# Kernel optimization log

Measured on AMD Instinct MI355X. Metric: run time of the kernel, lower is better.

The kernel has to match this reference:

```python
import jax, jax.numpy as jnp
import numpy as np

BQ = 64  # query block size
BK = 64  # key block size
PV_SCALE = 1e-3  # pvthreshd (~0..50) -> prob threshold, mirrors int8 P-quantization cutoff


def setup_inputs() -> dict:
    key = jax.random.key(0)
    ks = jax.random.split(key, 6)
    B, H, L, D = 2, 16, 2048, 64
    q = jax.random.normal(ks[0], (B, H, L, D), jnp.float32)
    k = jax.random.normal(ks[1], (B, H, L, D), jnp.float32)
    v = jax.random.normal(ks[2], (B, H, L, D), jnp.float32)
    # per-head tuned thresholds (init defaults / autotune ranges)
    cdfthreshd = 0.85 + 0.14 * jax.random.uniform(ks[3], (H,), jnp.float32)
    simthreshd1 = jax.random.uniform(ks[4], (H,), jnp.float32, minval=-0.3, maxval=0.5)
    pvthreshd = jax.random.uniform(ks[5], (H,), jnp.float32, minval=15.0, maxval=25.0)
    return dict(q=q, k=k, v=v, cdfthreshd=cdfthreshd,
                simthreshd1=simthreshd1, pvthreshd=pvthreshd)


def _sparse_meansim_attention(q, k, v, cdfthreshd, simthreshd1, pvthreshd):
    B, H, L, D = q.shape
    nqb, nkb = L // BQ, L // BK
    scale = 1.0 / jnp.sqrt(jnp.float32(D))

    # smooth_k: subtract per-(B,H) key mean along sequence
    k = k - k.mean(axis=2, keepdims=True)

    qb = q.reshape(B, H, nqb, BQ, D)
    kb = k.reshape(B, H, nkb, BK, D)
    qm = qb.mean(axis=3)  # [B,H,nqb,D]
    km = kb.mean(axis=3)  # [B,H,nkb,D]

    # mean cosine similarity of queries to their block mean -> pooled (prunable) blocks
    qn = jnp.linalg.norm(qb, axis=-1)            # [B,H,nqb,BQ]
    qmn = jnp.linalg.norm(qm, axis=-1)           # [B,H,nqb]
    cos = jnp.einsum('bhnqd,bhnd->bhnq', qb, qm) / (qn * qmn[..., None] + 1e-6)
    pooled = cos.mean(axis=-1) > simthreshd1[None, :, None]  # [B,H,nqb]

    # block-level score map from pooled means, CDF-based top-mass block selection
    s = jnp.einsum('bhid,bhjd->bhij', qm, km) * scale        # [B,H,nqb,nkb]
    p = jax.nn.softmax(s, axis=-1)
    order = jnp.argsort(-p, axis=-1)
    p_sorted = jnp.take_along_axis(p, order, axis=-1)
    excl_cdf = jnp.cumsum(p_sorted, axis=-1) - p_sorted      # exclusive CDF
    keep_sorted = excl_cdf < cdfthreshd[None, :, None, None]
    keep = jnp.take_along_axis(keep_sorted, jnp.argsort(order, axis=-1), axis=-1)

    sink = (jnp.arange(nkb) == 0)  # attention_sink: always keep first key block
    block_mask = keep | (~pooled)[..., None] | sink          # [B,H,nqb,nkb]

    # full attention restricted to selected blocks
    S = jnp.einsum('bhqd,bhkd->bhqk', q, k) * scale          # [B,H,L,L]
    m = jnp.repeat(jnp.repeat(block_mask, BQ, axis=2), BK, axis=3)
    P = jax.nn.softmax(jnp.where(m, S, -jnp.inf), axis=-1)

    # second-stage PV pruning: skip PV accumulation for negligible prob blocks
    Pb = P.reshape(B, H, nqb, BQ, nkb, BK)
    pv_keep = Pb.max(axis=(3, 5)) >= pvthreshd[None, :, None, None] * PV_SCALE
    pv_keep = pv_keep | sink
    Pb = Pb * pv_keep[:, :, :, None, :, None].astype(P.dtype)

    o = jnp.einsum('bhqk,bhkd->bhqd', Pb.reshape(B, H, L, L), v)
    return o


def reference(q, k, v, cdfthreshd, simthreshd1, pvthreshd):
    return _sparse_meansim_attention(q, k, v, cdfthreshd, simthreshd1, pvthreshd)
```

## Files before the change

kernel.cpp:

```cpp
#include <hip/hip_runtime.h>
#include <hip/hip_bf16.h>
#include <math.h>
#include <stdint.h>

#define B 2
#define H 16
#define L 2048
#define D 64
#define NB 32

typedef unsigned short u16;
typedef unsigned int u32;
typedef __attribute__((ext_vector_type(2))) unsigned int u32x2;
typedef __attribute__((ext_vector_type(4))) unsigned int u32x4;
typedef __attribute__((ext_vector_type(8))) short s16x8;
typedef __attribute__((ext_vector_type(4))) float f32x4;

union FragU { s16x8 v; u32 u[4]; };

__device__ __forceinline__ u32 pkbf(float a, float b) {
  __hip_bfloat162 h = __float22bfloat162_rn(make_float2(a, b));
  union { __hip_bfloat162 h; u32 u; } cv; cv.h = h; return cv.u;
}
__device__ __forceinline__ float bf2f(u32 u16bits) {
  union { u32 u; float f; } c; c.u = u16bits << 16; return c.f;
}
__device__ __forceinline__ void split4(float4 p, u32x2& hi, u32x2& lo) {
  u32 h01 = pkbf(p.x, p.y), h23 = pkbf(p.z, p.w);
  float rx = p.x - bf2f(h01 & 0xffffu);
  float ry = p.y - bf2f(h01 >> 16);
  float rz = p.z - bf2f(h23 & 0xffffu);
  float rw = p.w - bf2f(h23 >> 16);
  hi = (u32x2){h01, h23};
  lo = (u32x2){pkbf(rx, ry), pkbf(rz, rw)};
}
__device__ __forceinline__ int swz(int row, int colb) {
  return (row << 7) + (colb ^ ((row & 7) << 4));
}

__global__ __launch_bounds__(256) void k_prep(const float* __restrict__ k,
                                              const float* __restrict__ v,
                                              float* __restrict__ ksum,
                                              u16* __restrict__ khi_g,
                                              u16* __restrict__ klo_g,
                                              u16* __restrict__ vthi_g,
                                              u16* __restrict__ vtlo_g,
                                              float* __restrict__ kbmax) {
  int blk = blockIdx.x, bh = blk >> 5, j = blk & 31, t = threadIdx.x;
  int lane = t & 63, w = t >> 6;
  __shared__ float vt[64 * 65];
  __shared__ float pk_[4][64];
  __shared__ unsigned bmaxS;
  if (t == 0) bmaxS = 0u;
  size_t base = (size_t)blk * 4096;

  int r0 = t >> 3;
  int c8 = (t & 7) * 8;
  float cs[8] = {0.f, 0.f, 0.f, 0.f, 0.f, 0.f, 0.f, 0.f};
  float rmax = 0.f;
#pragma unroll
  for (int it = 0; it < 2; ++it) {
    int r = r0 + 32 * it;
    const float* kp = k + base + r * 64 + c8;
    float4 f0 = *(const float4*)kp;
    float4 f1 = *(const float4*)(kp + 4);
    u32x2 h0, l0, h1, l1;
    split4(f0, h0, l0); split4(f1, h1, l1);
    *(u32x4*)(khi_g + base + r * 64 + c8) = (u32x4){h0[0], h0[1], h1[0], h1[1]};
    *(u32x4*)(klo_g + base + r * 64 + c8) = (u32x4){l0[0], l0[1], l1[0], l1[1]};
    cs[0] += f0.x; cs[1] += f0.y; cs[2] += f0.z; cs[3] += f0.w;
    cs[4] += f1.x; cs[5] += f1.y; cs[6] += f1.z; cs[7] += f1.w;
    float ssq = f0.x*f0.x + f0.y*f0.y + f0.z*f0.z + f0.w*f0.w
              + f1.x*f1.x + f1.y*f1.y + f1.z*f1.z + f1.w*f1.w;
    ssq += __shfl_xor(ssq, 1); ssq += __shfl_xor(ssq, 2); ssq += __shfl_xor(ssq, 4);
    if ((t & 7) == 0) rmax = fmaxf(rmax, ssq);
    const float* vp = v + base + r * 64 + c8;
    float4 g0 = *(const float4*)vp;
    float4 g1 = *(const float4*)(vp + 4);
    vt[(c8 + 0) * 65 + r] = g0.x;
    vt[(c8 + 1) * 65 + r] = g0.y;
    vt[(c8 + 2) * 65 + r] = g0.z;
    vt[(c8 + 3) * 65 + r] = g0.w;
    vt[(c8 + 4) * 65 + r] = g1.x;
    vt[(c8 + 5) * 65 + r] = g1.y;
    vt[(c8 + 6) * 65 + r] = g1.z;
    vt[(c8 + 7) * 65 + r] = g1.w;
  }
  if ((t & 7) == 0) atomicMax(&bmaxS, __float_as_uint(rmax));
#pragma unroll
  for (int i = 0; i < 8; ++i) {
    cs[i] += __shfl_xor(cs[i], 8);
    cs[i] += __shfl_xor(cs[i], 16);
    cs[i] += __shfl_xor(cs[i], 32);
  }
  if (lane < 8) {
    *(float4*)&pk_[w][lane * 8]     = (float4){cs[0], cs[1], cs[2], cs[3]};
    *(float4*)&pk_[w][lane * 8 + 4] = (float4){cs[4], cs[5], cs[6], cs[7]};
  }
  __syncthreads();
  if (t < 64) ksum[(size_t)blk * 64 + t] = pk_[0][t] + pk_[1][t] + pk_[2][t] + pk_[3][t];
  if (t == 0) kbmax[blk] = __uint_as_float(bmaxS);
#pragma unroll
  for (int it = 0; it < 2; ++it) {
    int idx = t + 256 * it, d = idx >> 3, s8 = (idx & 7) * 8;
    const float* vr = &vt[d * 65 + s8];
    float4 f0 = {vr[0], vr[1], vr[2], vr[3]};
    float4 f1 = {vr[4], vr[5], vr[6], vr[7]};
    u32x2 h0, l0, h1, l1;
    split4(f0, h0, l0); split4(f1, h1, l1);
    size_t o = (size_t)bh * 131072 + (size_t)d * 2048 + j * 64 + s8;
    *(u32x4*)(vthi_g + o) = (u32x4){h0[0], h0[1], h1[0], h1[1]};
    *(u32x4*)(vtlo_g + o) = (u32x4){l0[0], l0[1], l1[0], l1[1]};
  }
}

__global__ __launch_bounds__(256, 3) void k_attn(
    const float* __restrict__ q,
    const float* __restrict__ ksum,
    const u16* __restrict__ khi_g, const u16* __restrict__ klo_g,
    const u16* __restrict__ vthi_g, const u16* __restrict__ vtlo_g,
    const float* __restrict__ cdfthreshd, const float* __restrict__ simthreshd1,
    const float* __restrict__ pvthreshd, const float* __restrict__ kbmax,
    float* __restrict__ out) {
  int blk0 = blockIdx.x;
  int blk = (blk0 & 7) * 128 + (blk0 >> 3);
  int bh = blk >> 5, iq = blk & 31, h = bh & (H - 1);
  int t = threadIdx.x, lane = t & 63, w = t >> 6;
  int m16 = lane & 15, quad = lane >> 4;

  __shared__ __align__(16) uint8_t smem[24608];
  uint8_t* phB = smem;
  uint8_t* plB = smem + 8192;
  uint8_t* qloB = smem + 16384;
  u32*   rbm   = (u32*)smem;
  float* lpart = (float*)(smem + 8448);
  float* qmS   = (float*)(smem + 9472);
  float* MSs   = (float*)(smem + 9728);
  float* linvS = (float*)(smem + 9984);
  int*   flg   = (int*)(smem + 24576);

  const float* qg = q + ((size_t)bh * L + (size_t)iq * 64) * D;
  const u16* kh = khi_g + (size_t)bh * (L * D);
  const u16* kl = klo_g + (size_t)bh * (L * D);
  const u16* vh = vthi_g + (size_t)bh * (L * D);
  const u16* vl = vtlo_g + (size_t)bh * (L * D);

  s16x8 qhf[4][2];
#pragma unroll
  for (int nt = 0; nt < 4; ++nt)
#pragma unroll
    for (int ks = 0; ks < 2; ++ks) {
      const float* p0 = qg + (size_t)(16 * nt + m16) * 64 + ks * 32 + quad * 8;
      float4 a = *(const float4*)p0;
      float4 b2 = *(const float4*)(p0 + 4);
      u32x2 ha, la, hb, lb;
      split4(a, ha, la); split4(b2, hb, lb);
      FragU fh;
      fh.u[0] = ha[0]; fh.u[1] = ha[1]; fh.u[2] = hb[0]; fh.u[3] = hb[1];
      qhf[nt][ks] = fh.v;
      if (w == 0)
        *(u32x4*)(qloB + swz(16 * nt + m16, ks * 64 + quad * 16)) =
            (u32x4){la[0], la[1], lb[0], lb[1]};
    }
  for (int e = t; e < 64 * 33; e += 256) rbm[e] = 0x7F800000u;

  if (w == 0) {
    float s = 0.f;
    for (int r = 0; r < 64; ++r) s += qg[r * 64 + lane];
    qmS[lane] = s * (1.f / 64.f);
  }
  if (w == 1) {
    float m = (lane < 32) ? kbmax[bh * 32 + lane] : 0.f;
    for (int off = 16; off; off >>= 1) m = fmaxf(m, __shfl_xor(m, off, 32));
    if (lane == 0) ((float*)flg)[3] = m;
  }
  __syncthreads();

  bool keepj = false;
  if (w == 0 && lane < 32) {
    int j = lane;
    const float* ksp = ksum + (size_t)bh * NB * 64 + j * 64;
    float sv = 0.f;
    for (int d = 0; d < 64; ++d) sv += qmS[d] * ksp[d];
    sv *= (1.f / 64.f) * 0.125f;
    float mx = sv;
    for (int off = 16; off; off >>= 1) mx = fmaxf(mx, __shfl_xor(mx, off, 32));
    float p = expf(sv - mx);
    float sum = p;
    for (int off = 16; off; off >>= 1) sum += __shfl_xor(sum, off, 32);
    p /= sum;
    float excl = 0.f;
    for (int u = 0; u < 32; ++u) {
      float pu = __shfl(p, u, 32);
      if ((pu > p) || (pu == p && u < j)) excl += pu;
    }
    keepj = excl < cdfthreshd[h];
  }
  if (w == 1) {
    int r = lane;
    float kmax2 = ((float*)flg)[3];
    float dot = 0.f, qn2 = 0.f, qmn2 = 0.f;
    for (int d = 0; d < 64; ++d) {
      float a = qg[r * 64 + d], b2 = qmS[d];
      dot += a * b2; qn2 += a * a; qmn2 += b2 * b2;
    }
    float cs = dot / (sqrtf(qn2) * sqrtf(qmn2) + 1e-6f);
    float su = cs;
    for (int off = 32; off; off >>= 1) su += __shfl_xor(su, off);
    if (lane == 0) flg[0] = (su * (1.f / 64.f)) > simthreshd1[h];
    MSs[r] = sqrtf(qn2 * kmax2) * 0.125f;
  }
  __syncthreads();
  if (w == 0 && lane < 32) {
    bool bit = keepj || !flg[0] || (lane == 0);
    unsigned long long bal = __ballot(bit);
    if (lane == 0) flg[1] = (int)(u32)bal;
  }
  __syncthreads();
  u32 mw = (u32)flg[1];

  float Mq[4];
#pragma unroll
  for (int nt = 0; nt < 4; ++nt) Mq[nt] = MSs[16 * nt + m16];

  float lp[4] = {0.f, 0.f, 0.f, 0.f};
  {
    u32 rm = mw;
    int j = (int)__builtin_ctz(rm); rm &= rm - 1;
    s16x8 ka0[2], ka1[2];
    {
      const u16* kr0 = kh + (size_t)(j * 64 + 16 * w + m16) * 64 + quad * 8;
      const u16* kl0 = kl + (size_t)(j * 64 + 16 * w + m16) * 64 + quad * 8;
#pragma unroll
      for (int ks = 0; ks < 2; ++ks) {
        ka0[ks] = *(const s16x8*)(kr0 + ks * 32);
        ka1[ks] = *(const s16x8*)(kl0 + ks * 32);
      }
    }
    for (;;) {
      f32x4 acc[4];
#pragma unroll
      for (int nt = 0; nt < 4; ++nt) acc[nt] = (f32x4){0.f, 0.f, 0.f, 0.f};
#pragma unroll
      for (int ks = 0; ks < 2; ++ks) {
        s16x8 ql_[4];
#pragma unroll
        for (int nt = 0; nt < 4; ++nt)
          ql_[nt] = *(const s16x8*)(qloB + swz(16 * nt + m16, ks * 64 + quad * 16));
        __builtin_amdgcn_s_setprio(1);
#pragma unroll
        for (int nt = 0; nt < 4; ++nt) {
          acc[nt] = __builtin_amdgcn_mfma_f32_16x16x32_bf16(ka0[ks], qhf[nt][ks], acc[nt], 0, 0, 0);
          acc[nt] = __builtin_amdgcn_mfma_f32_16x16x32_bf16(ka1[ks], qhf[nt][ks], acc[nt], 0, 0, 0);
          acc[nt] = __builtin_amdgcn_mfma_f32_16x16x32_bf16(ka0[ks], ql_[nt], acc[nt], 0, 0, 0);
        }
        __builtin_amdgcn_s_setprio(0);
      }
      int nj = -1;
      s16x8 kn0[2], kn1[2];
      if (rm) {
        nj = (int)__builtin_ctz(rm); rm &= rm - 1;
        const u16* nr = kh + (size_t)(nj * 64 + 16 * w + m16) * 64 + quad * 8;
        const u16* nl = kl + (size_t)(nj * 64 + 16 * w + m16) * 64 + quad * 8;
#pragma unroll
        for (int ks = 0; ks < 2; ++ks) {
          kn0[ks] = *(const s16x8*)(nr + ks * 32);
          kn1[ks] = *(const s16x8*)(nl + ks * 32);
        }
      }
#pragma unroll
      for (int nt = 0; nt < 4; ++nt) {
        float vmax = -1e30f;
#pragma unroll
        for (int reg = 0; reg < 4; ++reg) {
          float s = acc[nt][reg] * 0.125f - Mq[nt];
          lp[nt] += __expf(s);
          vmax = fmaxf(vmax, s);
        }
        vmax = fmaxf(vmax, __shfl_xor(vmax, 16));
        vmax = fmaxf(vmax, __shfl_xor(vmax, 32));
        if (quad == 0)
          atomicMin(rbm + (16 * nt + m16) * 33 + j, __float_as_uint(fmaxf(-vmax, 0.f)));
      }
      if (nj < 0) break;
#pragma unroll
      for (int ks = 0; ks < 2; ++ks) { ka0[ks] = kn0[ks]; ka1[ks] = kn1[ks]; }
      j = nj;
    }
  }
#pragma unroll
  for (int nt = 0; nt < 4; ++nt) {
    float s = lp[nt];
    s += __shfl_xor(s, 16); s += __shfl_xor(s, 32);
    if (quad == 0) lpart[w * 64 + 16 * nt + m16] = s;
  }
  __syncthreads();
  if (t < 64) linvS[t] = 1.f / (lpart[t] + lpart[64 + t] + lpart[128 + t] + lpart[192 + t]);
  __syncthreads();

  if (w == 0 && lane < 32) {
    bool keep = (mw >> lane) & 1u;
    if (keep && lane != 0) {
      float thr = pvthreshd[h] * 1e-3f;
      float mp = 0.f;
      for (int r = 0; r < 64; ++r) {
        float key = __uint_as_float(rbm[r * 33 + lane]);
        mp = fmaxf(mp, __expf(-key) * linvS[r]);
      }
      keep = mp >= thr;
    }
    unsigned long long bal = __ballot(keep);
    if (lane == 0) flg[2] = (int)(u32)bal;
  }
  __syncthreads();
  u32 gm = (u32)flg[2];

  float linq[4];
#pragma unroll
  for (int nt = 0; nt < 4; ++nt) linq[nt] = linvS[16 * nt + m16];

  f32x4 oacc[4];
#pragma unroll
  for (int nt = 0; nt < 4; ++nt) oacc[nt] = (f32x4){0.f, 0.f, 0.f, 0.f};
  {
    u32 rg = gm;
    int j = (int)__builtin_ctz(rg); rg &= rg - 1;
    s16x8 ka0[2], ka1[2];
    {
      const u16* kr0 = kh + (size_t)(j * 64 + 16 * w + m16) * 64 + quad * 8;
      const u16* kl0 = kl + (size_t)(j * 64 + 16 * w + m16) * 64 + quad * 8;
#pragma unroll
      for (int ks = 0; ks < 2; ++ks) {
        ka0[ks] = *(const s16x8*)(kr0 + ks * 32);
        ka1[ks] = *(const s16x8*)(kl0 + ks * 32);
      }
    }
    for (;;) {
      f32x4 acc[4];
#pragma unroll
      for (int nt = 0; nt < 4; ++nt) acc[nt] = (f32x4){0.f, 0.f, 0.f, 0.f};
#pragma unroll
      for (int ks = 0; ks < 2; ++ks) {
        s16x8 ql_[4];
#pragma unroll
        for (int nt = 0; nt < 4; ++nt)
          ql_[nt] = *(const s16x8*)(qloB + swz(16 * nt + m16, ks * 64 + quad * 16));
        __builtin_amdgcn_s_setprio(1);
#pragma unroll
        for (int nt = 0; nt < 4; ++nt) {
          acc[nt] = __builtin_amdgcn_mfma_f32_16x16x32_bf16(ka0[ks], qhf[nt][ks], acc[nt], 0, 0, 0);
          acc[nt] = __builtin_amdgcn_mfma_f32_16x16x32_bf16(ka1[ks], qhf[nt][ks], acc[nt], 0, 0, 0);
          acc[nt] = __builtin_amdgcn_mfma_f32_16x16x32_bf16(ka0[ks], ql_[nt], acc[nt], 0, 0, 0);
        }
        __builtin_amdgcn_s_setprio(0);
      }
      int nj = -1;
      s16x8 kn0[2], kn1[2];
      if (rg) {
        nj = (int)__builtin_ctz(rg); rg &= rg - 1;
        const u16* nr = kh + (size_t)(nj * 64 + 16 * w + m16) * 64 + quad * 8;
        const u16* nl = kl + (size_t)(nj * 64 + 16 * w + m16) * 64 + quad * 8;
#pragma unroll
        for (int ks = 0; ks < 2; ++ks) {
          kn0[ks] = *(const s16x8*)(nr + ks * 32);
          kn1[ks] = *(const s16x8*)(nl + ks * 32);
        }
      }
      __syncthreads();
#pragma unroll
      for (int nt = 0; nt < 4; ++nt) {
        float4 pv;
        pv.x = __expf(acc[nt][0] * 0.125f - Mq[nt]) * linq[nt];
        pv.y = __expf(acc[nt][1] * 0.125f - Mq[nt]) * linq[nt];
        pv.z = __expf(acc[nt][2] * 0.125f - Mq[nt]) * linq[nt];
        pv.w = __expf(acc[nt][3] * 0.125f - Mq[nt]) * linq[nt];
        u32x2 hi, lo; split4(pv, hi, lo);
        int off = swz(16 * nt + m16, 32 * w + 8 * quad);
        *(u32x2*)(phB + off) = hi;
        *(u32x2*)(plB + off) = lo;
      }
      s16x8 va0[2], va1[2];
      {
        const u16* vr0 = vh + (size_t)(16 * w + m16) * L + j * 64 + quad * 8;
        const u16* vl0 = vl + (size_t)(16 * w + m16) * L + j * 64 + quad * 8;
#pragma unroll
        for (int ks = 0; ks < 2; ++ks) {
          va0[ks] = *(const s16x8*)(vr0 + ks * 32);
          va1[ks] = *(const s16x8*)(vl0 + ks * 32);
        }
      }
      __syncthreads();
#pragma unroll
      for (int ks = 0; ks < 2; ++ks)
#pragma unroll
        for (int nt = 0; nt < 4; ++nt) {
          s16x8 pbh = *(const s16x8*)(phB + swz(16 * nt + m16, ks * 64 + quad * 16));
          s16x8 pbl = *(const s16x8*)(plB + swz(16 * nt + m16, ks * 64 + quad * 16));
          __builtin_amdgcn_s_setprio(1);
          oacc[nt] = __builtin_amdgcn_mfma_f32_16x16x32_bf16(va0[ks], pbh, oacc[nt], 0, 0, 0);
          oacc[nt] = __builtin_amdgcn_mfma_f32_16x16x32_bf16(va1[ks], pbh, oacc[nt], 0, 0, 0);
          oacc[nt] = __builtin_amdgcn_mfma_f32_16x16x32_bf16(va0[ks], pbl, oacc[nt], 0, 0, 0);
          __builtin_amdgcn_s_setprio(0);
        }
      if (nj < 0) break;
#pragma unroll
      for (int ks = 0; ks < 2; ++ks) { ka0[ks] = kn0[ks]; ka1[ks] = kn1[ks]; }
      j = nj;
    }
  }

  float* ob = out + ((size_t)bh * L + (size_t)iq * 64) * D;
#pragma unroll
  for (int nt = 0; nt < 4; ++nt)
    *(f32x4*)(ob + (size_t)(16 * nt + m16) * 64 + 16 * w + 4 * quad) = oacc[nt];
}

extern "C" void kernel_launch(void* const* d_in, const int* in_sizes, int n_in,
                              void* d_out, int out_size, void* d_ws, size_t ws_size,
                              hipStream_t stream) {
  (void)in_sizes; (void)n_in; (void)out_size; (void)ws_size;
  const float* q   = (const float*)d_in[0];
  const float* k   = (const float*)d_in[1];
  const float* v   = (const float*)d_in[2];
  const float* cdf = (const float*)d_in[3];
  const float* sim = (const float*)d_in[4];
  const float* pvt = (const float*)d_in[5];
  float* out = (float*)d_out;

  uint8_t* w8 = (uint8_t*)d_ws;
  float* ksum  = (float*)w8;
  float* kbmax = (float*)(w8 + 262144);
  u16* khi_g  = (u16*)(w8 + 266240);
  u16* klo_g  = khi_g + (size_t)B * H * L * D;
  u16* vthi_g = klo_g + (size_t)B * H * L * D;
  u16* vtlo_g = vthi_g + (size_t)B * H * L * D;

  k_prep<<<B * H * NB, 256, 0, stream>>>(k, v, ksum, khi_g, klo_g, vthi_g, vtlo_g, kbmax);
  k_attn<<<B * H * NB, 256, 0, stream>>>(q, ksum, khi_g, klo_g, vthi_g, vtlo_g,
                                         cdf, sim, pvt, kbmax, out);
}
```

Baseline: 215.5 us.

## Double-buffer P tiles, keep Q-lo in registers, use exp2, remap prep blocks

The PV loop now double-buffers the P hi/lo tiles in shared memory, so each iteration needs one barrier instead of two. V loads are issued at the top of the iteration to overlap with the QK MFMAs. Q low-part fragments stay in registers instead of being reread from LDS, and exponentials become exp2 with the scale folded into a single fma. Other changes: the prep kernel's block order is remapped per XCD, output uses nontemporal stores, and k_attn's launch_bounds minimum occupancy drops from 3 to 2, which allows more registers but may cost occupancy.

Measured after the change: 210.4 us. 1.02x faster.

```diff
diff --git a/kernel.cpp b/kernel.cpp
--- a/kernel.cpp
+++ b/kernel.cpp
@@ -17,6 +17,18 @@
 typedef __attribute__((ext_vector_type(4))) float f32x4;
 
 union FragU { s16x8 v; u32 u[4]; };
+
+#if defined(__has_builtin)
+#if __has_builtin(__builtin_amdgcn_exp2f)
+#define EXP2F __builtin_amdgcn_exp2f
+#else
+#define EXP2F exp2f
+#endif
+#else
+#define EXP2F exp2f
+#endif
+#define LOG2E 1.4426950408889634f
+#define C1SC 0.18033688011112042f
 
 __device__ __forceinline__ u32 pkbf(float a, float b) {
   __hip_bfloat162 h = __float22bfloat162_rn(make_float2(a, b));
@@ -46,7 +58,10 @@
                                               u16* __restrict__ vthi_g,
                                               u16* __restrict__ vtlo_g,
                                               float* __restrict__ kbmax) {
-  int blk = blockIdx.x, bh = blk >> 5, j = blk & 31, t = threadIdx.x;
+  int blk0 = blockIdx.x, t = threadIdx.x;
+  int xcd = blk0 & 7, sidx = blk0 >> 3;
+  int bh = xcd * 4 + (sidx >> 5), j = sidx & 31;
+  int blk = bh * 32 + j;
   int lane = t & 63, w = t >> 6;
   __shared__ float vt[64 * 65];
   __shared__ float pk_[4][64];
@@ -114,7 +129,7 @@
   }
 }
 
-__global__ __launch_bounds__(256, 3) void k_attn(
+__global__ __launch_bounds__(256, 2) void k_attn(
     const float* __restrict__ q,
     const float* __restrict__ ksum,
     const u16* __restrict__ khi_g, const u16* __restrict__ klo_g,
@@ -128,16 +143,15 @@
   int t = threadIdx.x, lane = t & 63, w = t >> 6;
   int m16 = lane & 15, quad = lane >> 4;
 
-  __shared__ __align__(16) uint8_t smem[24608];
-  uint8_t* phB = smem;
-  uint8_t* plB = smem + 8192;
-  uint8_t* qloB = smem + 16384;
+  __shared__ __align__(16) uint8_t smem[32800];
   u32*   rbm   = (u32*)smem;
   float* lpart = (float*)(smem + 8448);
   float* qmS   = (float*)(smem + 9472);
   float* MSs   = (float*)(smem + 9728);
   float* linvS = (float*)(smem + 9984);
-  int*   flg   = (int*)(smem + 24576);
+  int*   flg   = (int*)(smem + 32768);
+#define PHB(b) (smem + (b) * 16384)
+#define PLB(b) (smem + (b) * 16384 + 8192)
 
   const float* qg = q + ((size_t)bh * L + (size_t)iq * 64) * D;
   const u16* kh = khi_g + (size_t)bh * (L * D);
@@ -145,22 +159,20 @@
   const u16* vh = vthi_g + (size_t)bh * (L * D);
   const u16* vl = vtlo_g + (size_t)bh * (L * D);
 
-  s16x8 qhf[4][2];
+  s16x8 qhf[4][2], qlf[4][2];
 #pragma unroll
   for (int nt = 0; nt < 4; ++nt)
 #pragma unroll
     for (int ks = 0; ks < 2; ++ks) {
-      const float* p0 = qg + (size_t)(16 * nt + m16) * 64 + ks * 32 + quad * 8;
+      const float* p0 = qg + (16 * nt + m16) * 64 + ks * 32 + quad * 8;
       float4 a = *(const float4*)p0;
       float4 b2 = *(const float4*)(p0 + 4);
       u32x2 ha, la, hb, lb;
       split4(a, ha, la); split4(b2, hb, lb);
-      FragU fh;
+      FragU fh, fl;
       fh.u[0] = ha[0]; fh.u[1] = ha[1]; fh.u[2] = hb[0]; fh.u[3] = hb[1];
-      qhf[nt][ks] = fh.v;
-      if (w == 0)
-        *(u32x4*)(qloB + swz(16 * nt + m16, ks * 64 + quad * 16)) =
-            (u32x4){la[0], la[1], lb[0], lb[1]};
+      fl.u[0] = la[0]; fl.u[1] = la[1]; fl.u[2] = lb[0]; fl.u[3] = lb[1];
+      qhf[nt][ks] = fh.v; qlf[nt][ks] = fl.v;
     }
   for (int e = t; e < 64 * 33; e += 256) rbm[e] = 0x7F800000u;
 
@@ -221,7 +233,7 @@
 
   float Mq[4];
 #pragma unroll
-  for (int nt = 0; nt < 4; ++nt) Mq[nt] = MSs[16 * nt + m16];
+  for (int nt = 0; nt < 4; ++nt) Mq[nt] = MSs[16 * nt + m16] * LOG2E;
 
   float lp[4] = {0.f, 0.f, 0.f, 0.f};
   {
@@ -241,21 +253,16 @@
       f32x4 acc[4];
 #pragma unroll
       for (int nt = 0; nt < 4; ++nt) acc[nt] = (f32x4){0.f, 0.f, 0.f, 0.f};
-#pragma unroll
-      for (int ks = 0; ks < 2; ++ks) {
-        s16x8 ql_[4];
-#pragma unroll
-        for (int nt = 0; nt < 4; ++nt)
-          ql_[nt] = *(const s16x8*)(qloB + swz(16 * nt + m16, ks * 64 + quad * 16));
-        __builtin_amdgcn_s_setprio(1);
+      __builtin_amdgcn_s_setprio(1);
+#pragma unroll
+      for (int ks = 0; ks < 2; ++ks)
 #pragma unroll
         for (int nt = 0; nt < 4; ++nt) {
           acc[nt] = __builtin_amdgcn_mfma_f32_16x16x32_bf16(ka0[ks], qhf[nt][ks], acc[nt], 0, 0, 0);
           acc[nt] = __builtin_amdgcn_mfma_f32_16x16x32_bf16(ka1[ks], qhf[nt][ks], acc[nt], 0, 0, 0);
-          acc[nt] = __builtin_amdgcn_mfma_f32_16x16x32_bf16(ka0[ks], ql_[nt], acc[nt], 0, 0, 0);
-        }
-        __builtin_amdgcn_s_setprio(0);
-      }
+          acc[nt] = __builtin_amdgcn_mfma_f32_16x16x32_bf16(ka0[ks], qlf[nt][ks], acc[nt], 0, 0, 0);
+        }
+      __builtin_amdgcn_s_setprio(0);
       int nj = -1;
       s16x8 kn0[2], kn1[2];
       if (rm) {
@@ -273,8 +280,8 @@
         float vmax = -1e30f;
 #pragma unroll
         for (int reg = 0; reg < 4; ++reg) {
-          float s = acc[nt][reg] * 0.125f - Mq[nt];
-          lp[nt] += __expf(s);
+          float s = fmaf(acc[nt][reg], C1SC, -Mq[nt]);
+          lp[nt] += EXP2F(s);
           vmax = fmaxf(vmax, s);
         }
         vmax = fmaxf(vmax, __shfl_xor(vmax, 16));
@@ -305,7 +312,7 @@
       float mp = 0.f;
       for (int r = 0; r < 64; ++r) {
         float key = __uint_as_float(rbm[r * 33 + lane]);
-        mp = fmaxf(mp, __expf(-key) * linvS[r]);
+        mp = fmaxf(mp, EXP2F(-key) * linvS[r]);
       }
       keep = mp >= thr;
     }
@@ -318,13 +325,15 @@
   float linq[4];
 #pragma unroll
   for (int nt = 0; nt < 4; ++nt) linq[nt] = linvS[16 * nt + m16];
-
   f32x4 oacc[4];
 #pragma unroll
   for (int nt = 0; nt < 4; ++nt) oacc[nt] = (f32x4){0.f, 0.f, 0.f, 0.f};
+  __syncthreads();
+
   {
     u32 rg = gm;
     int j = (int)__builtin_ctz(rg); rg &= rg - 1;
+    int buf = 0;
     s16x8 ka0[2], ka1[2];
     {
       const u16* kr0 = kh + (size_t)(j * 64 + 16 * w + m16) * 64 + quad * 8;
@@ -336,66 +345,61 @@
       }
     }
     for (;;) {
+      s16x8 va0[2], va1[2];
+      {
+        const u16* vr0 = vh + (size_t)(16 * w + m16) * L + j * 64 + quad * 8;
+        const u16* vl0 = vl + (size_t)(16 * w + m16) * L + j * 64 + quad * 8;
+#pragma unroll
+        for (int ks = 0; ks < 2; ++ks) {
+          va0[ks] = *(const s16x8*)(vr0 + ks * 32);
+          va1[ks] = *(const s16x8*)(vl0 + ks * 32);
+        }
+      }
       f32x4 acc[4];
 #pragma unroll
       for (int nt = 0; nt < 4; ++nt) acc[nt] = (f32x4){0.f, 0.f, 0.f, 0.f};
-#pragma unroll
-      for (int ks = 0; ks < 2; ++ks) {
-        s16x8 ql_[4];
-#pragma unroll
-        for (int nt = 0; nt < 4; ++nt)
-          ql_[nt] = *(const s16x8*)(qloB + swz(16 * nt + m16, ks * 64 + quad * 16));
-        __builtin_amdgcn_s_setprio(1);
+      __builtin_amdgcn_s_setprio(1);
+#pragma unroll
+      for (int ks = 0; ks < 2; ++ks)
 #pragma unroll
         for (int nt = 0; nt < 4; ++nt) {
           acc[nt] = __builtin_amdgcn_mfma_f32_16x16x32_bf16(ka0[ks], qhf[nt][ks], acc[nt], 0, 0, 0);
           acc[nt] = __builtin_amdgcn_mfma_f32_16x16x32_bf16(ka1[ks], qhf[nt][ks], acc[nt], 0, 0, 0);
-          acc[nt] = __builtin_amdgcn_mfma_f32_16x16x32_bf16(ka0[ks], ql_[nt], acc[nt], 0, 0, 0);
-        }
-        __builtin_amdgcn_s_setprio(0);
+          acc[nt] = __builtin_amdgcn_mfma_f32_16x16x32_bf16(ka0[ks], qlf[nt][ks], acc[nt], 0, 0, 0);
+        }
+      __builtin_amdgcn_s_setprio(0);
+#pragma unroll
+      for (int nt = 0; nt < 4; ++nt) {
+        float4 pv;
+        pv.x = EXP2F(fmaf(acc[nt][0], C1SC, -Mq[nt])) * linq[nt];
+        pv.y = EXP2F(fmaf(acc[nt][1], C1SC, -Mq[nt])) * linq[nt];
+        pv.z = EXP2F(fmaf(acc[nt][2], C1SC, -Mq[nt])) * linq[nt];
+        pv.w = EXP2F(fmaf(acc[nt][3], C1SC, -Mq[nt])) * linq[nt];
+        u32x2 hi, lo; split4(pv, hi, lo);
+        int off = swz(16 * nt + m16, 32 * w + 8 * quad);
+        *(u32x2*)(PHB(buf) + off) = hi;
+        *(u32x2*)(PLB(buf) + off) = lo;
       }
       int nj = -1;
-      s16x8 kn0[2], kn1[2];
       if (rg) {
         nj = (int)__builtin_ctz(rg); rg &= rg - 1;
         const u16* nr = kh + (size_t)(nj * 64 + 16 * w + m16) * 64 + quad * 8;
         const u16* nl = kl + (size_t)(nj * 64 + 16 * w + m16) * 64 + quad * 8;
 #pragma unroll
         for (int ks = 0; ks < 2; ++ks) {
-          kn0[ks] = *(const s16x8*)(nr + ks * 32);
-          kn1[ks] = *(const s16x8*)(nl + ks * 32);
+          ka0[ks] = *(const s16x8*)(nr + ks * 32);
+          ka1[ks] = *(const s16x8*)(nl + ks * 32);
         }
       }
       __syncthreads();
-#pragma unroll
-      for (int nt = 0; nt < 4; ++nt) {
-        float4 pv;
-        pv.x = __expf(acc[nt][0] * 0.125f - Mq[nt]) * linq[nt];
-        pv.y = __expf(acc[nt][1] * 0.125f - Mq[nt]) * linq[nt];
-        pv.z = __expf(acc[nt][2] * 0.125f - Mq[nt]) * linq[nt];
-        pv.w = __expf(acc[nt][3] * 0.125f - Mq[nt]) * linq[nt];
-        u32x2 hi, lo; split4(pv, hi, lo);
-        int off = swz(16 * nt + m16, 32 * w + 8 * quad);
-        *(u32x2*)(phB + off) = hi;
-        *(u32x2*)(plB + off) = lo;
-      }
-      s16x8 va0[2], va1[2];
-      {
-        const u16* vr0 = vh + (size_t)(16 * w + m16) * L + j * 64 + quad * 8;
-        const u16* vl0 = vl + (size_t)(16 * w + m16) * L + j * 64 + quad * 8;
-#pragma unroll
-        for (int ks = 0; ks < 2; ++ks) {
-          va0[ks] = *(const s16x8*)(vr0 + ks * 32);
-          va1[ks] = *(const s16x8*)(vl0 + ks * 32);
-        }
-      }
-      __syncthreads();
+      const uint8_t* ph_ = PHB(buf);
+      const uint8_t* pl_ = PLB(buf);
 #pragma unroll
       for (int ks = 0; ks < 2; ++ks)
 #pragma unroll
         for (int nt = 0; nt < 4; ++nt) {
-          s16x8 pbh = *(const s16x8*)(phB + swz(16 * nt + m16, ks * 64 + quad * 16));
-          s16x8 pbl = *(const s16x8*)(plB + swz(16 * nt + m16, ks * 64 + quad * 16));
+          s16x8 pbh = *(const s16x8*)(ph_ + swz(16 * nt + m16, ks * 64 + quad * 16));
+          s16x8 pbl = *(const s16x8*)(pl_ + swz(16 * nt + m16, ks * 64 + quad * 16));
           __builtin_amdgcn_s_setprio(1);
           oacc[nt] = __builtin_amdgcn_mfma_f32_16x16x32_bf16(va0[ks], pbh, oacc[nt], 0, 0, 0);
           oacc[nt] = __builtin_amdgcn_mfma_f32_16x16x32_bf16(va1[ks], pbh, oacc[nt], 0, 0, 0);
@@ -403,8 +407,7 @@
           __builtin_amdgcn_s_setprio(0);
         }
       if (nj < 0) break;
-#pragma unroll
-      for (int ks = 0; ks < 2; ++ks) { ka0[ks] = kn0[ks]; ka1[ks] = kn1[ks]; }
+      buf ^= 1;
       j = nj;
     }
   }
@@ -412,7 +415,8 @@
   float* ob = out + ((size_t)bh * L + (size_t)iq * 64) * D;
 #pragma unroll
   for (int nt = 0; nt < 4; ++nt)
-    *(f32x4*)(ob + (size_t)(16 * nt + m16) * 64 + 16 * w + 4 * quad) = oacc[nt];
+    __builtin_nontemporal_store(oacc[nt],
+        (f32x4*)(ob + (16 * nt + m16) * 64 + 16 * w + 4 * quad));
 }
 
 extern "C" void kernel_launch(void* const* d_in, const int* in_sizes, int n_in,
```
